# Optimization experiments

Hardware: AMD Instinct MI355X
Metric: run time of the kernel (lower is better)

The kernel has to match this reference:

```python
import jax, jax.numpy as jnp
import numpy as np

B, S, NQ, H, HD = 2, 4096, 576, 32, 128
HID = H * HD  # 4096


def setup_inputs() -> dict:
    key = jax.random.key(0)
    ks = jax.random.split(key, 7)
    sc = 0.02
    return {
        "hidden_states": jax.random.normal(ks[0], (B, S, HID), jnp.float32),
        "by_pass_hidden_states": jax.random.normal(ks[1], (B, NQ, HID), jnp.float32),
        "attention_mask": jnp.zeros((B, 1, S, NQ), jnp.float32),
        "Wq": jax.random.normal(ks[2], (HID, HID), jnp.float32) * sc,
        "Wk": jax.random.normal(ks[3], (HID, HID), jnp.float32) * sc,
        "Wv": jax.random.normal(ks[4], (HID, HID), jnp.float32) * sc,
        "Wo": jax.random.normal(ks[5], (HID, HID), jnp.float32) * sc,
    }


def reference(hidden_states, by_pass_hidden_states, attention_mask, Wq, Wk, Wv, Wo):
    b, s, _ = hidden_states.shape
    nq = by_pass_hidden_states.shape[1]
    # projections (nn.Linear applies x @ W.T); reshape to (b, heads, len, head_dim)
    q = (hidden_states @ Wq.T).reshape(b, s, H, HD).transpose(0, 2, 1, 3)
    k = (by_pass_hidden_states @ Wk.T).reshape(b, nq, H, HD).transpose(0, 2, 1, 3)
    v = (by_pass_hidden_states @ Wv.T).reshape(b, nq, H, HD).transpose(0, 2, 1, 3)
    # eager QK^T -> mask -> fp32 softmax -> V
    scores = jnp.einsum("bhsd,bhqd->bhsq", q, k) / jnp.sqrt(jnp.float32(HD))
    scores = scores + attention_mask  # (b,1,s,nq) broadcast over heads
    attn = jax.nn.softmax(scores.astype(jnp.float32), axis=-1).astype(q.dtype)
    out = jnp.einsum("bhsq,bhqd->bhsd", attn, v)
    out = out.transpose(0, 2, 1, 3).reshape(b, s, HID)
    return out @ Wo.T
```

## Files before the change

kernel.cpp:

```cpp
#include <hip/hip_runtime.h>
#include <stdint.h>

#define Bn   2
#define Sn   4096
#define NQn  576
#define Hn   32
#define HDn  128
#define HIDn 4096

typedef unsigned short bfu;
typedef short short8 __attribute__((ext_vector_type(8)));
typedef float f32x4 __attribute__((ext_vector_type(4)));

__device__ __forceinline__ bfu f2b(float f) {
  uint32_t x = __builtin_bit_cast(uint32_t, f);
  return (bfu)((x + 0x7fffu + ((x >> 16) & 1u)) >> 16);
}

__device__ __forceinline__ void gload16(const void* g, void* l) {
  __builtin_amdgcn_global_load_lds(
      (const __attribute__((address_space(1))) uint32_t*)g,
      (__attribute__((address_space(3))) uint32_t*)l, 16, 0, 0);
}

__global__ void cast_f32_bf16(const float* __restrict__ in, bfu* __restrict__ out,
                              int n8) {
  int i = blockIdx.x * 256 + threadIdx.x;
  if (i >= n8) return;
  const float4* in4 = (const float4*)in;
  float4 a = in4[2 * i], c = in4[2 * i + 1];
  short8 v;
  v[0] = (short)f2b(a.x); v[1] = (short)f2b(a.y);
  v[2] = (short)f2b(a.z); v[3] = (short)f2b(a.w);
  v[4] = (short)f2b(c.x); v[5] = (short)f2b(c.y);
  v[6] = (short)f2b(c.z); v[7] = (short)f2b(c.w);
  ((short8*)out)[i] = v;
}

template <int WRITE_BF16>
__global__ __launch_bounds__(512, 2)
void gemm_bt256(const bfu* __restrict__ A, const bfu* __restrict__ Bm,
                void* __restrict__ Cout, int M, int N, int K) {
  __shared__ __align__(16) bfu Asm[2][256 * 64];
  __shared__ __align__(16) bfu Bsm[2][256 * 64];
  const int tid = threadIdx.x;
  const int wave = tid >> 6, lane = tid & 63;
  const int lr = lane & 15, kq = lane >> 4;
  const int wm = wave >> 2, wn = wave & 3;
  const long m0 = (long)blockIdx.y * 256, n0 = (long)blockIdx.x * 256;
  const int NT = K >> 6;

  const int c0j = tid >> 3, c0c = tid & 7;
  const int c1j = (512 + tid) >> 3, c1c = tid & 7;
  const bfu* aSrc0 = A + (m0 + c0j) * (long)K + ((c0c ^ (c0j & 7)) * 8);
  const bfu* aSrc1 = A + (m0 + c1j) * (long)K + ((c1c ^ (c1j & 7)) * 8);
  const bfu* bSrc0 = Bm + (n0 + c0j) * (long)K + ((c0c ^ (c0j & 7)) * 8);
  const bfu* bSrc1 = Bm + (n0 + c1j) * (long)K + ((c1c ^ (c1j & 7)) * 8);

  auto stageA = [&](int t, int buf, int half) {
    long koff = (long)t * 64 + (long)half * 128 * K;
    gload16(aSrc0 + koff, &Asm[buf][half * 8192 + (wave * 64) * 8]);
    gload16(aSrc1 + koff, &Asm[buf][half * 8192 + (512 + wave * 64) * 8]);
  };
  auto stageB = [&](int t, int buf, int half) {
    long koff = (long)t * 64 + (long)half * 128 * K;
    gload16(bSrc0 + koff, &Bsm[buf][half * 8192 + (wave * 64) * 8]);
    gload16(bSrc1 + koff, &Bsm[buf][half * 8192 + (512 + wave * 64) * 8]);
  };
  auto ldsA = [&](int buf, int mf, int ks) -> short8 {
    int row = (mf >> 2) * 128 + wm * 64 + (mf & 3) * 16 + lr;
    int off = (row * 128 + ks * 64 + kq * 16) ^ ((row & 7) << 4);
    return *(const short8*)((const char*)Asm[buf] + off);
  };
  auto ldsB = [&](int buf, int nf, int ks) -> short8 {
    int row = (nf >> 1) * 128 + wn * 32 + (nf & 1) * 16 + lr;
    int off = (row * 128 + ks * 64 + kq * 16) ^ ((row & 7) << 4);
    return *(const short8*)((const char*)Bsm[buf] + off);
  };

  f32x4 acc[8][4] = {};

  stageA(0, 0, 0); stageB(0, 0, 0); stageB(0, 0, 1); stageA(0, 0, 1);
  asm volatile("s_waitcnt vmcnt(0)" ::: "memory");
  __builtin_amdgcn_s_barrier();

  for (int t = 0; t < NT; ++t) {
    const int buf = t & 1;
    if (t + 1 < NT) {
      stageA(t + 1, buf ^ 1, 0);
      stageB(t + 1, buf ^ 1, 0);
      stageB(t + 1, buf ^ 1, 1);
      stageA(t + 1, buf ^ 1, 1);
    }
    short8 a0[4][2], a1[4][2], b0[2][2], b1[2][2];
#pragma unroll
    for (int mf = 0; mf < 4; ++mf) {
      a0[mf][0] = ldsA(buf, mf, 0);
      a0[mf][1] = ldsA(buf, mf, 1);
    }
#pragma unroll
    for (int nf = 0; nf < 2; ++nf) {
      b0[nf][0] = ldsB(buf, nf, 0);
      b0[nf][1] = ldsB(buf, nf, 1);
      b1[nf][0] = ldsB(buf, 2 + nf, 0);
      b1[nf][1] = ldsB(buf, 2 + nf, 1);
    }
#pragma unroll
    for (int mf = 0; mf < 4; ++mf)
#pragma unroll
      for (int ks = 0; ks < 2; ++ks)
#pragma unroll
        for (int nf = 0; nf < 2; ++nf)
          acc[mf][nf] = __builtin_amdgcn_mfma_f32_16x16x32_bf16(
              a0[mf][ks], b0[nf][ks], acc[mf][nf], 0, 0, 0);
#pragma unroll
    for (int mf = 0; mf < 4; ++mf) {
      a1[mf][0] = ldsA(buf, 4 + mf, 0);
      a1[mf][1] = ldsA(buf, 4 + mf, 1);
    }
#pragma unroll
    for (int mf = 0; mf < 4; ++mf)
#pragma unroll
      for (int ks = 0; ks < 2; ++ks)
#pragma unroll
        for (int nf = 0; nf < 2; ++nf)
          acc[mf][2 + nf] = __builtin_amdgcn_mfma_f32_16x16x32_bf16(
              a0[mf][ks], b1[nf][ks], acc[mf][2 + nf], 0, 0, 0);
#pragma unroll
    for (int mf = 0; mf < 4; ++mf)
#pragma unroll
      for (int ks = 0; ks < 2; ++ks)
#pragma unroll
        for (int nf = 0; nf < 2; ++nf)
          acc[4 + mf][2 + nf] = __builtin_amdgcn_mfma_f32_16x16x32_bf16(
              a1[mf][ks], b1[nf][ks], acc[4 + mf][2 + nf], 0, 0, 0);
#pragma unroll
    for (int mf = 0; mf < 4; ++mf)
#pragma unroll
      for (int ks = 0; ks < 2; ++ks)
#pragma unroll
        for (int nf = 0; nf < 2; ++nf)
          acc[4 + mf][nf] = __builtin_amdgcn_mfma_f32_16x16x32_bf16(
              a1[mf][ks], b0[nf][ks], acc[4 + mf][nf], 0, 0, 0);
    asm volatile("s_waitcnt vmcnt(0)" ::: "memory");
    __builtin_amdgcn_s_barrier();
  }

#pragma unroll
  for (int mf = 0; mf < 8; ++mf)
#pragma unroll
    for (int nf = 0; nf < 4; ++nf)
#pragma unroll
      for (int r = 0; r < 4; ++r) {
        long row = m0 + (mf >> 2) * 128 + wm * 64 + (mf & 3) * 16 + kq * 4 + r;
        long col = n0 + (nf >> 1) * 128 + wn * 32 + (nf & 1) * 16 + lr;
        float v = acc[mf][nf][r];
        if (WRITE_BF16)
          ((bfu*)Cout)[row * N + col] = f2b(v);
        else
          ((float*)Cout)[row * N + col] = v;
      }
}

template <int WRITE_BF16>
__global__ __launch_bounds__(256, 2)
void gemm_bt(const bfu* __restrict__ A, const bfu* __restrict__ Bm,
             void* __restrict__ Cout, int M, int N, int K) {
  __shared__ __align__(16) bfu As[128 * 32];
  __shared__ __align__(16) bfu Bs[128 * 32];
  const int tid = threadIdx.x;
  const int wave = tid >> 6, lane = tid & 63;
  const int lr = lane & 15, kq = lane >> 4;
  const int wm = wave >> 1, wn = wave & 1;
  const long m0 = (long)blockIdx.y * 128, n0 = (long)blockIdx.x * 128;

  f32x4 acc[4][4] = {};

  for (int kk = 0; kk < K; kk += 32) {
#pragma unroll
    for (int i = 0; i < 2; ++i) {
      int tt = i * 256 + tid;
      long row = tt >> 2;
      int col = (tt & 3) * 8;
      gload16(A + (m0 + row) * K + kk + col, &As[(i * 256 + wave * 64) * 8]);
      gload16(Bm + (n0 + row) * K + kk + col, &Bs[(i * 256 + wave * 64) * 8]);
    }
    __syncthreads();
    short8 a[4], b[4];
#pragma unroll
    for (int mt = 0; mt < 4; ++mt)
      a[mt] = *(const short8*)&As[(wm * 64 + mt * 16 + lr) * 32 + kq * 8];
#pragma unroll
    for (int nt = 0; nt < 4; ++nt)
      b[nt] = *(const short8*)&Bs[(wn * 64 + nt * 16 + lr) * 32 + kq * 8];
#pragma unroll
    for (int mt = 0; mt < 4; ++mt)
#pragma unroll
      for (int nt = 0; nt < 4; ++nt)
        acc[mt][nt] = __builtin_amdgcn_mfma_f32_16x16x32_bf16(
            a[mt], b[nt], acc[mt][nt], 0, 0, 0);
    __syncthreads();
  }
#pragma unroll
  for (int mt = 0; mt < 4; ++mt)
#pragma unroll
    for (int nt = 0; nt < 4; ++nt)
#pragma unroll
      for (int r = 0; r < 4; ++r) {
        long row = m0 + wm * 64 + mt * 16 + kq * 4 + r;
        long col = n0 + wn * 64 + nt * 16 + lr;
        float v = acc[mt][nt][r];
        if (WRITE_BF16)
          ((bfu*)Cout)[row * N + col] = f2b(v);
        else
          ((float*)Cout)[row * N + col] = v;
      }
}

__global__ void transpose_v(const bfu* __restrict__ KVb, bfu* __restrict__ Vt) {
  __shared__ bfu t[32][33];
  const int bh = blockIdx.z;
  const int tq = blockIdx.x;
  const int td = blockIdx.y;
  const int b = bh >> 5, h = bh & 31;
  const int tx = threadIdx.x & 31, ty = threadIdx.x >> 5;
  const bfu* src =
      KVb + ((long)(b * NQn + tq * 32)) * 8192 + 4096 + h * HDn + td * 32;
#pragma unroll
  for (int i = 0; i < 32; i += 8) t[ty + i][tx] = src[(long)(ty + i) * 8192 + tx];
  __syncthreads();
  bfu* dst = Vt + ((long)bh * HDn + td * 32) * NQn + tq * 32;
#pragma unroll
  for (int i = 0; i < 32; i += 8) dst[(long)(ty + i) * NQn + tx] = t[tx][ty + i];
}

__global__ __launch_bounds__(256, 4)
void attn_kernel(const bfu* __restrict__ Qb, const bfu* __restrict__ KVb,
                 const bfu* __restrict__ Vt, const float* __restrict__ mask,
                 bfu* __restrict__ AO) {
  __shared__ __align__(16) bfu Ks[2][4096];
  __shared__ __align__(16) bfu Vs[2][4096];
  const int bid = blockIdx.x;
  const int h = bid & (Hn - 1);
  const int b = (bid >> 5) & (Bn - 1);
  const int qt0 = bid >> 6;
  const long q0 = (long)qt0 * 64;
  const int tid = threadIdx.x;
  const int wave = tid >> 6, lane = tid & 63;
  const int lr = lane & 15, kq = lane >> 4;
  const float scale = 0.08838834764831845f;

  const long qrow = (long)b * Sn + q0 + wave * 16 + lr;
  const bfu* Kblk = KVb + (long)b * NQn * 8192 + h * HDn;
  const bfu* Vblk = Vt + ((long)(b * Hn + h)) * HDn * NQn;
  const float* mrow = mask + ((long)b * Sn + q0 + wave * 16 + lr) * NQn;

  auto stageK = [&](int kt, int buf) {
#pragma unroll
    for (int i = 0; i < 2; ++i) {
      int c = i * 256 + tid;
      int j = c >> 4, c16 = c & 15;
      gload16(Kblk + (long)(kt * 32 + j) * 8192 + ((c16 ^ (j & 7)) * 8),
              &Ks[buf][(i * 256 + wave * 64) * 8]);
    }
  };
  auto stageV = [&](int kt, int buf) {
#pragma unroll
    for (int i = 0; i < 2; ++i) {
      int c = i * 256 + tid;
      int j = c >> 2, c4 = c & 3;
      gload16(Vblk + (long)j * NQn + kt * 32 + c4 * 8,
              &Vs[buf][(i * 256 + wave * 64) * 8]);
    }
  };

  stageK(0, 0);
  stageV(0, 0);

  const bfu* Qbase = Qb + qrow * HIDn + h * HDn;
  short8 qf[4];
#pragma unroll
  for (int ks = 0; ks < 4; ++ks)
    qf[ks] = *(const short8*)&Qbase[ks * 32 + kq * 8];

  f32x4 o[8] = {};
  float rsum = 0.f;

  for (int kt = 0; kt < 18; ++kt) {
    __syncthreads();
    const int buf = kt & 1;
    if (kt < 17) {
      stageK(kt + 1, buf ^ 1);
      stageV(kt + 1, buf ^ 1);
    }
    const char* kb = (const char*)Ks[buf];
    f32x4 s0 = {}, s1 = {};
#pragma unroll
    for (int ks = 0; ks < 4; ++ks) {
      short8 kf0 = *(const short8*)(kb + ((lr * 256 + ks * 64 + kq * 16) ^
                                          ((lr & 7) << 4)));
      short8 kf1 = *(const short8*)(kb + (((16 + lr) * 256 + ks * 64 + kq * 16) ^
                                          ((lr & 7) << 4)));
      s0 = __builtin_amdgcn_mfma_f32_16x16x32_bf16(kf0, qf[ks], s0, 0, 0, 0);
      s1 = __builtin_amdgcn_mfma_f32_16x16x32_bf16(kf1, qf[ks], s1, 0, 0, 0);
    }
    float4 m0 = *(const float4*)&mrow[kt * 32 + kq * 4];
    float4 m1 = *(const float4*)&mrow[kt * 32 + 16 + kq * 4];
    float p00 = __expf(s0[0] * scale + m0.x), p01 = __expf(s0[1] * scale + m0.y);
    float p02 = __expf(s0[2] * scale + m0.z), p03 = __expf(s0[3] * scale + m0.w);
    float p10 = __expf(s1[0] * scale + m1.x), p11 = __expf(s1[1] * scale + m1.y);
    float p12 = __expf(s1[2] * scale + m1.z), p13 = __expf(s1[3] * scale + m1.w);
    rsum += ((p00 + p01) + (p02 + p03)) + ((p10 + p11) + (p12 + p13));
    int pk0_0 = (int)((uint32_t)f2b(p00) | ((uint32_t)f2b(p01) << 16));
    int pk0_1 = (int)((uint32_t)f2b(p02) | ((uint32_t)f2b(p03) << 16));
    int pk1_0 = (int)((uint32_t)f2b(p10) | ((uint32_t)f2b(p11) << 16));
    int pk1_1 = (int)((uint32_t)f2b(p12) | ((uint32_t)f2b(p13) << 16));
    const int sLo = lr + (((kq & 1) << 1) << 4);
    const int sHi = sLo + 16;
    int b0, b1, b2, b3;
    {
      int v0 = __shfl(pk0_0, sLo, 64), v1 = __shfl(pk1_0, sLo, 64);
      b0 = (kq < 2) ? v0 : v1;
      v0 = __shfl(pk0_1, sLo, 64); v1 = __shfl(pk1_1, sLo, 64);
      b1 = (kq < 2) ? v0 : v1;
      v0 = __shfl(pk0_0, sHi, 64); v1 = __shfl(pk1_0, sHi, 64);
      b2 = (kq < 2) ? v0 : v1;
      v0 = __shfl(pk0_1, sHi, 64); v1 = __shfl(pk1_1, sHi, 64);
      b3 = (kq < 2) ? v0 : v1;
    }
    int4 pfi = {b0, b1, b2, b3};
    short8 pfrag = __builtin_bit_cast(short8, pfi);
    const char* vb = (const char*)Vs[buf];
#pragma unroll
    for (int dt = 0; dt < 8; ++dt) {
      short8 vf = *(const short8*)(vb + ((dt * 16 + lr) * 64 + kq * 16));
      o[dt] = __builtin_amdgcn_mfma_f32_16x16x32_bf16(vf, pfrag, o[dt], 0, 0, 0);
    }
  }

  rsum += __shfl_xor(rsum, 16, 64);
  rsum += __shfl_xor(rsum, 32, 64);
  const float inv = 1.0f / rsum;

  bfu* Obase = AO + qrow * HIDn + h * HDn;
#pragma unroll
  for (int dt = 0; dt < 8; ++dt) {
    uint64_t pk = (uint64_t)f2b(o[dt][0] * inv) |
                  ((uint64_t)f2b(o[dt][1] * inv) << 16) |
                  ((uint64_t)f2b(o[dt][2] * inv) << 32) |
                  ((uint64_t)f2b(o[dt][3] * inv) << 48);
    *(uint64_t*)&Obase[dt * 16 + kq * 4] = pk;
  }
}

extern "C" void kernel_launch(void* const* d_in, const int* in_sizes, int n_in,
                              void* d_out, int out_size, void* d_ws, size_t ws_size,
                              hipStream_t stream) {
  const float* hs = (const float*)d_in[0];
  const float* bp = (const float*)d_in[1];
  const float* mask = (const float*)d_in[2];
  const float* Wq = (const float*)d_in[3];
  const float* Wk = (const float*)d_in[4];
  const float* Wv = (const float*)d_in[5];
  const float* Wo = (const float*)d_in[6];
  float* out = (float*)d_out;

  const long M1 = (long)Bn * Sn;
  const long M2 = (long)Bn * NQn;
  char* ws = (char*)d_ws;
  bfu* hb = (bfu*)(ws + 0);
  bfu* bb = (bfu*)(ws + 67108864);
  bfu* w1 = (bfu*)(ws + 76546048);
  bfu* wkv = (bfu*)(ws + 110100480);
  bfu* Qb = (bfu*)(ws + 177209344);
  bfu* KVb = (bfu*)(ws + 244318208);
  bfu* Vt = (bfu*)(ws + 263192576);

  auto cast = [&](const float* src, bfu* dst, long n) {
    int n8 = (int)(n / 8);
    cast_f32_bf16<<<dim3((n8 + 255) / 256), dim3(256), 0, stream>>>(src, dst, n8);
  };
  cast(hs, hb, M1 * HIDn);
  cast(bp, bb, M2 * HIDn);
  cast(Wq, w1, (long)HIDn * HIDn);
  cast(Wk, wkv, (long)HIDn * HIDn);
  cast(Wv, wkv + (long)HIDn * HIDn, (long)HIDn * HIDn);

  gemm_bt256<1><<<dim3(HIDn / 256, M1 / 256), dim3(512), 0, stream>>>(
      hb, w1, Qb, (int)M1, HIDn, HIDn);
  gemm_bt<1><<<dim3(8192 / 128, M2 / 128), dim3(256), 0, stream>>>(
      bb, wkv, KVb, (int)M2, 8192, HIDn);

  cast(Wo, w1, (long)HIDn * HIDn);
  transpose_v<<<dim3(NQn / 32, HDn / 32, Bn * Hn), dim3(256), 0, stream>>>(
      KVb, Vt);

  attn_kernel<<<dim3((Sn / 64) * Bn * Hn), dim3(256), 0, stream>>>(
      Qb, KVb, Vt, mask, hb );

  gemm_bt256<0><<<dim3(HIDn / 256, M1 / 256), dim3(512), 0, stream>>>(
      hb, w1, out, (int)M1, HIDn, HIDn);
}
```

Before: 902.7 us.

## Replace double-buffered LDS staging with single buffer in GEMM

```diff
diff --git a/kernel.cpp b/kernel.cpp
--- a/kernel.cpp
+++ b/kernel.cpp
@@ -41,8 +41,8 @@
 __global__ __launch_bounds__(512, 2)
 void gemm_bt256(const bfu* __restrict__ A, const bfu* __restrict__ Bm,
                 void* __restrict__ Cout, int M, int N, int K) {
-  __shared__ __align__(16) bfu Asm[2][256 * 64];
-  __shared__ __align__(16) bfu Bsm[2][256 * 64];
+  __shared__ __align__(16) bfu Asm[256 * 64];
+  __shared__ __align__(16) bfu Bsm[256 * 64];
   const int tid = threadIdx.x;
   const int wave = tid >> 6, lane = tid & 63;
   const int lr = lane & 15, kq = lane >> 4;
@@ -57,53 +57,45 @@
   const bfu* bSrc0 = Bm + (n0 + c0j) * (long)K + ((c0c ^ (c0j & 7)) * 8);
   const bfu* bSrc1 = Bm + (n0 + c1j) * (long)K + ((c1c ^ (c1j & 7)) * 8);
 
-  auto stageA = [&](int t, int buf, int half) {
+  auto stageA = [&](int t, int half) {
     long koff = (long)t * 64 + (long)half * 128 * K;
-    gload16(aSrc0 + koff, &Asm[buf][half * 8192 + (wave * 64) * 8]);
-    gload16(aSrc1 + koff, &Asm[buf][half * 8192 + (512 + wave * 64) * 8]);
-  };
-  auto stageB = [&](int t, int buf, int half) {
+    gload16(aSrc0 + koff, &Asm[half * 8192 + (wave * 64) * 8]);
+    gload16(aSrc1 + koff, &Asm[half * 8192 + (512 + wave * 64) * 8]);
+  };
+  auto stageB = [&](int t, int half) {
     long koff = (long)t * 64 + (long)half * 128 * K;
-    gload16(bSrc0 + koff, &Bsm[buf][half * 8192 + (wave * 64) * 8]);
-    gload16(bSrc1 + koff, &Bsm[buf][half * 8192 + (512 + wave * 64) * 8]);
-  };
-  auto ldsA = [&](int buf, int mf, int ks) -> short8 {
+    gload16(bSrc0 + koff, &Bsm[half * 8192 + (wave * 64) * 8]);
+    gload16(bSrc1 + koff, &Bsm[half * 8192 + (512 + wave * 64) * 8]);
+  };
+  auto ldsA = [&](int mf, int ks) -> short8 {
     int row = (mf >> 2) * 128 + wm * 64 + (mf & 3) * 16 + lr;
     int off = (row * 128 + ks * 64 + kq * 16) ^ ((row & 7) << 4);
-    return *(const short8*)((const char*)Asm[buf] + off);
-  };
-  auto ldsB = [&](int buf, int nf, int ks) -> short8 {
+    return *(const short8*)((const char*)Asm + off);
+  };
+  auto ldsB = [&](int nf, int ks) -> short8 {
     int row = (nf >> 1) * 128 + wn * 32 + (nf & 1) * 16 + lr;
     int off = (row * 128 + ks * 64 + kq * 16) ^ ((row & 7) << 4);
-    return *(const short8*)((const char*)Bsm[buf] + off);
+    return *(const short8*)((const char*)Bsm + off);
   };
 
   f32x4 acc[8][4] = {};
 
-  stageA(0, 0, 0); stageB(0, 0, 0); stageB(0, 0, 1); stageA(0, 0, 1);
-  asm volatile("s_waitcnt vmcnt(0)" ::: "memory");
-  __builtin_amdgcn_s_barrier();
-
   for (int t = 0; t < NT; ++t) {
-    const int buf = t & 1;
-    if (t + 1 < NT) {
-      stageA(t + 1, buf ^ 1, 0);
-      stageB(t + 1, buf ^ 1, 0);
-      stageB(t + 1, buf ^ 1, 1);
-      stageA(t + 1, buf ^ 1, 1);
-    }
+    stageA(t, 0); stageB(t, 0); stageB(t, 1); stageA(t, 1);
+    asm volatile("s_waitcnt vmcnt(0)" ::: "memory");
+    __builtin_amdgcn_s_barrier();
     short8 a0[4][2], a1[4][2], b0[2][2], b1[2][2];
 #pragma unroll
     for (int mf = 0; mf < 4; ++mf) {
-      a0[mf][0] = ldsA(buf, mf, 0);
-      a0[mf][1] = ldsA(buf, mf, 1);
+      a0[mf][0] = ldsA(mf, 0);
+      a0[mf][1] = ldsA(mf, 1);
     }
 #pragma unroll
     for (int nf = 0; nf < 2; ++nf) {
-      b0[nf][0] = ldsB(buf, nf, 0);
-      b0[nf][1] = ldsB(buf, nf, 1);
-      b1[nf][0] = ldsB(buf, 2 + nf, 0);
-      b1[nf][1] = ldsB(buf, 2 + nf, 1);
+      b0[nf][0] = ldsB(nf, 0);
+      b0[nf][1] = ldsB(nf, 1);
+      b1[nf][0] = ldsB(2 + nf, 0);
+      b1[nf][1] = ldsB(2 + nf, 1);
     }
 #pragma unroll
     for (int mf = 0; mf < 4; ++mf)
@@ -115,8 +107,8 @@
               a0[mf][ks], b0[nf][ks], acc[mf][nf], 0, 0, 0);
 #pragma unroll
     for (int mf = 0; mf < 4; ++mf) {
-      a1[mf][0] = ldsA(buf, 4 + mf, 0);
-      a1[mf][1] = ldsA(buf, 4 + mf, 1);
+      a1[mf][0] = ldsA(4 + mf, 0);
+      a1[mf][1] = ldsA(4 + mf, 1);
     }
 #pragma unroll
     for (int mf = 0; mf < 4; ++mf)
@@ -142,7 +134,6 @@
         for (int nf = 0; nf < 2; ++nf)
           acc[4 + mf][nf] = __builtin_amdgcn_mfma_f32_16x16x32_bf16(
               a1[mf][ks], b0[nf][ks], acc[4 + mf][nf], 0, 0, 0);
-    asm volatile("s_waitcnt vmcnt(0)" ::: "memory");
     __builtin_amdgcn_s_barrier();
   }
 
```

After: 974.6 us. 8.0% more time.

## Restructure GEMM main loop into 8-wave ping-pong schedule with interleaved prefetch

Applied to the files above, without the earlier changes.

```diff
diff --git a/kernel.cpp b/kernel.cpp
--- a/kernel.cpp
+++ b/kernel.cpp
@@ -79,72 +79,81 @@
   };
 
   f32x4 acc[8][4] = {};
+  short8 a0[4][2], a1[4][2], b0[2][2], b1[2][2];
+
+#define MFMA16(MB, NB, AA, BB)                                                  \
+  _Pragma("unroll") for (int mf = 0; mf < 4; ++mf)                              \
+      _Pragma("unroll") for (int ks = 0; ks < 2; ++ks)                          \
+      _Pragma("unroll") for (int nf = 0; nf < 2; ++nf)                          \
+      acc[MB + mf][NB + nf] = __builtin_amdgcn_mfma_f32_16x16x32_bf16(          \
+          AA[mf][ks], BB[nf][ks], acc[MB + mf][NB + nf], 0, 0, 0);
 
   stageA(0, 0, 0); stageB(0, 0, 0); stageB(0, 0, 1); stageA(0, 0, 1);
-  asm volatile("s_waitcnt vmcnt(0)" ::: "memory");
+  stageA(1, 1, 0); stageB(1, 1, 0); stageB(1, 1, 1); stageA(1, 1, 1);
+  asm volatile("s_waitcnt vmcnt(6)" ::: "memory");
   __builtin_amdgcn_s_barrier();
 
-  for (int t = 0; t < NT; ++t) {
-    const int buf = t & 1;
-    if (t + 1 < NT) {
-      stageA(t + 1, buf ^ 1, 0);
-      stageB(t + 1, buf ^ 1, 0);
-      stageB(t + 1, buf ^ 1, 1);
-      stageA(t + 1, buf ^ 1, 1);
-    }
-    short8 a0[4][2], a1[4][2], b0[2][2], b1[2][2];
-#pragma unroll
-    for (int mf = 0; mf < 4; ++mf) {
-      a0[mf][0] = ldsA(buf, mf, 0);
-      a0[mf][1] = ldsA(buf, mf, 1);
-    }
-#pragma unroll
-    for (int nf = 0; nf < 2; ++nf) {
-      b0[nf][0] = ldsB(buf, nf, 0);
-      b0[nf][1] = ldsB(buf, nf, 1);
-      b1[nf][0] = ldsB(buf, 2 + nf, 0);
-      b1[nf][1] = ldsB(buf, 2 + nf, 1);
-    }
-#pragma unroll
-    for (int mf = 0; mf < 4; ++mf)
-#pragma unroll
-      for (int ks = 0; ks < 2; ++ks)
-#pragma unroll
-        for (int nf = 0; nf < 2; ++nf)
-          acc[mf][nf] = __builtin_amdgcn_mfma_f32_16x16x32_bf16(
-              a0[mf][ks], b0[nf][ks], acc[mf][nf], 0, 0, 0);
-#pragma unroll
-    for (int mf = 0; mf < 4; ++mf) {
-      a1[mf][0] = ldsA(buf, 4 + mf, 0);
-      a1[mf][1] = ldsA(buf, 4 + mf, 1);
-    }
-#pragma unroll
-    for (int mf = 0; mf < 4; ++mf)
-#pragma unroll
-      for (int ks = 0; ks < 2; ++ks)
-#pragma unroll
-        for (int nf = 0; nf < 2; ++nf)
-          acc[mf][2 + nf] = __builtin_amdgcn_mfma_f32_16x16x32_bf16(
-              a0[mf][ks], b1[nf][ks], acc[mf][2 + nf], 0, 0, 0);
-#pragma unroll
-    for (int mf = 0; mf < 4; ++mf)
-#pragma unroll
-      for (int ks = 0; ks < 2; ++ks)
-#pragma unroll
-        for (int nf = 0; nf < 2; ++nf)
-          acc[4 + mf][2 + nf] = __builtin_amdgcn_mfma_f32_16x16x32_bf16(
-              a1[mf][ks], b1[nf][ks], acc[4 + mf][2 + nf], 0, 0, 0);
-#pragma unroll
-    for (int mf = 0; mf < 4; ++mf)
-#pragma unroll
-      for (int ks = 0; ks < 2; ++ks)
-#pragma unroll
-        for (int nf = 0; nf < 2; ++nf)
-          acc[4 + mf][nf] = __builtin_amdgcn_mfma_f32_16x16x32_bf16(
-              a1[mf][ks], b0[nf][ks], acc[4 + mf][nf], 0, 0, 0);
-    asm volatile("s_waitcnt vmcnt(0)" ::: "memory");
-    __builtin_amdgcn_s_barrier();
+  for (int tp = 0; tp < NT; tp += 2) {
+    const bool more = (tp + 2 < NT);
+#pragma unroll
+    for (int hh = 0; hh < 2; ++hh) {
+      const int bb = hh;
+      const int ts = tp + hh + 2;
+#pragma unroll
+      for (int mf = 0; mf < 4; ++mf) {
+        a0[mf][0] = ldsA(bb, mf, 0);
+        a0[mf][1] = ldsA(bb, mf, 1);
+      }
+#pragma unroll
+      for (int nf = 0; nf < 2; ++nf) {
+        b0[nf][0] = ldsB(bb, nf, 0);
+        b0[nf][1] = ldsB(bb, nf, 1);
+      }
+      asm volatile("s_waitcnt lgkmcnt(8)" ::: "memory");
+      __builtin_amdgcn_s_barrier();
+      asm volatile("s_waitcnt lgkmcnt(0)" ::: "memory");
+      __builtin_amdgcn_s_setprio(1);
+      MFMA16(0, 0, a0, b0)
+      __builtin_amdgcn_s_setprio(0);
+      __builtin_amdgcn_s_barrier();
+#pragma unroll
+      for (int nf = 0; nf < 2; ++nf) {
+        b1[nf][0] = ldsB(bb, 2 + nf, 0);
+        b1[nf][1] = ldsB(bb, 2 + nf, 1);
+      }
+      if (more) { stageA(ts, bb, 0); stageB(ts, bb, 0); }
+      __builtin_amdgcn_s_barrier();
+      asm volatile("s_waitcnt lgkmcnt(0)" ::: "memory");
+      __builtin_amdgcn_s_setprio(1);
+      MFMA16(0, 2, a0, b1)
+      __builtin_amdgcn_s_setprio(0);
+      __builtin_amdgcn_s_barrier();
+#pragma unroll
+      for (int mf = 0; mf < 4; ++mf) {
+        a1[mf][0] = ldsA(bb, 4 + mf, 0);
+        a1[mf][1] = ldsA(bb, 4 + mf, 1);
+      }
+      if (more) stageB(ts, bb, 1);
+      __builtin_amdgcn_s_barrier();
+      asm volatile("s_waitcnt lgkmcnt(0)" ::: "memory");
+      __builtin_amdgcn_s_setprio(1);
+      MFMA16(4, 2, a1, b1)
+      __builtin_amdgcn_s_setprio(0);
+      __builtin_amdgcn_s_barrier();
+      if (more) stageA(ts, bb, 1);
+      __builtin_amdgcn_s_barrier();
+      __builtin_amdgcn_s_setprio(1);
+      MFMA16(4, 0, a1, b0)
+      __builtin_amdgcn_s_setprio(0);
+      if (more) {
+        asm volatile("s_waitcnt vmcnt(6)" ::: "memory");
+      } else if (hh == 0) {
+        asm volatile("s_waitcnt vmcnt(0)" ::: "memory");
+      }
+      __builtin_amdgcn_s_barrier();
+    }
   }
+#undef MFMA16
 
 #pragma unroll
   for (int mf = 0; mf < 8; ++mf)
```

Result: no change. 896.4 us (-0.7%).
